# Kernel tuning notes

Hardware: AMD Instinct MI355X
Metric: run time of the kernel (lower is better)

The kernel has to match this reference:

```python
import jax, jax.numpy as jnp
import numpy as np
from jax import lax

B, L, E = 2, 2048, 1024          # batch, seq_len, embed_dim
NL = 2                            # n_layers
DI = 2 * E                        # d_inner (expand=2)
DS = 16                           # d_state
DC = 4                            # d_conv
DTR = (E + 15) // 16              # dt_rank = ceil(d_model/16) = 64


def setup_inputs() -> dict:
    key = jax.random.key(0)
    ks = jax.random.split(key, 12)
    s = 0.02
    inp = {
        "x": jax.random.normal(ks[0], (B, L, E), jnp.float32),
        "pos_embed": jax.random.normal(ks[1], (L, E), jnp.float32) * s,
        "in_proj_w": jax.random.normal(ks[2], (NL, 2 * DI, E), jnp.float32) * s,
        "conv_w": jax.random.normal(ks[3], (NL, DI, DC), jnp.float32) * s,
        "conv_b": jnp.zeros((NL, DI), jnp.float32),
        "x_proj_w": jax.random.normal(ks[4], (NL, DTR + 2 * DS, DI), jnp.float32) * s,
        "dt_proj_w": jax.random.normal(ks[5], (NL, DI, DTR), jnp.float32) * s,
        "dt_bias": jax.random.normal(ks[6], (NL, DI), jnp.float32) * 0.1,
        "A_log": jnp.broadcast_to(jnp.log(jnp.arange(1, DS + 1, dtype=jnp.float32)), (NL, DI, DS)) + 0.0,
        "D_skip": jnp.ones((NL, DI), jnp.float32),
        "out_proj_w": jax.random.normal(ks[7], (NL, E, DI), jnp.float32) * s,
        "norm_w": jnp.ones((NL, E), jnp.float32),
    }
    return inp


def _rmsnorm(x, w, eps=1e-6):
    return x * lax.rsqrt(jnp.mean(x * x, axis=-1, keepdims=True) + eps) * w


def _mamba(h, in_w, cw, cb, xw, dtw, dtb, A_log, Dp, ow):
    # h: (B, L, E)
    xz = jnp.einsum("ble,de->bld", h, in_w)          # (B, L, 2*DI)
    xc, z = jnp.split(xz, 2, axis=-1)                 # each (B, L, DI)
    # causal depthwise conv1d (kernel DC)
    xp = jnp.pad(xc, ((0, 0), (DC - 1, 0), (0, 0)))
    xconv = cb
    acc = jnp.zeros_like(xc)
    for k in range(DC):
        acc = acc + cw[:, k] * xp[:, k:k + xc.shape[1], :]
    xc = jax.nn.silu(acc + cb)
    # input-dependent SSM params
    x_dbl = jnp.einsum("bld,rd->blr", xc, xw)         # (B, L, DTR+2*DS)
    dt, Bm, C = jnp.split(x_dbl, [DTR, DTR + DS], axis=-1)
    delta = jax.nn.softplus(jnp.einsum("blr,dr->bld", dt, dtw) + dtb)  # (B, L, DI)
    A = -jnp.exp(A_log)                               # (DI, DS)

    def step(hst, inp):
        d, bm, c, u = inp                             # (B,DI),(B,DS),(B,DS),(B,DI)
        hst = jnp.exp(d[..., None] * A) * hst + (d * u)[..., None] * bm[:, None, :]
        y = jnp.einsum("bdn,bn->bd", hst, c)
        return hst, y

    h0 = jnp.zeros((h.shape[0], DI, DS), h.dtype)
    _, ys = lax.scan(step, h0, (delta.swapaxes(0, 1), Bm.swapaxes(0, 1),
                                C.swapaxes(0, 1), xc.swapaxes(0, 1)))
    y = ys.swapaxes(0, 1) + xc * Dp                   # (B, L, DI)
    y = y * jax.nn.silu(z)
    return jnp.einsum("bld,ed->ble", y, ow)


def reference(x, pos_embed, in_proj_w, conv_w, conv_b, x_proj_w, dt_proj_w,
              dt_bias, A_log, D_skip, out_proj_w, norm_w):
    h = x + pos_embed[None, :x.shape[1]]
    for i in range(in_proj_w.shape[0]):
        y = _mamba(h, in_proj_w[i], conv_w[i], conv_b[i], x_proj_w[i],
                   dt_proj_w[i], dt_bias[i], A_log[i], D_skip[i], out_proj_w[i])
        h = _rmsnorm(y + h, norm_w[i])
    return h
```

## Files before the change

### kernel.cpp

```cpp
#include <hip/hip_runtime.h>

#define B_   2
#define L_   2048
#define E_   1024
#define NL_  2
#define DI_  2048
#define DS_  16
#define DC_  4
#define DTR_ 64
#define NXD_ 96
#define M_   (B_ * L_)
#define NCH_ 64
#define LC_  32

typedef __attribute__((ext_vector_type(8))) short bf16x8;
typedef __attribute__((ext_vector_type(4))) float f32x4;

__device__ __forceinline__ float bf2f(unsigned short u) {
    return __uint_as_float(((unsigned)u) << 16);
}
__device__ __forceinline__ unsigned short f2bf(float f) {
    unsigned u = __float_as_uint(f);
    u += 0x7fff + ((u >> 16) & 1);
    return (unsigned short)(u >> 16);
}

#define LOG2E_ 1.44269504f
#define LN2_   0.69314718f

__device__ __forceinline__ float sigmoidf_(float x) {
    return __builtin_amdgcn_rcpf(1.f + __builtin_amdgcn_exp2f(-x * LOG2E_));
}
__device__ __forceinline__ float softplusf_(float x) {
    float e = __builtin_amdgcn_exp2f(x * LOG2E_);
    float s = LN2_ * __builtin_amdgcn_logf(1.f + e);
    return x > 15.f ? x : s;
}
__device__ __forceinline__ float expf_(float x) {
    return __builtin_amdgcn_exp2f(x * LOG2E_);
}
__device__ __forceinline__ float ldin(const void* p, size_t i, int isbf) {
    return isbf ? bf2f(((const unsigned short*)p)[i]) : ((const float*)p)[i];
}
__device__ __forceinline__ void gld_lds16(const unsigned short* g, unsigned short* l) {
    __builtin_amdgcn_global_load_lds(
        (const __attribute__((address_space(1))) unsigned int*)g,
        (__attribute__((address_space(3))) unsigned int*)l, 16, 0, 0);
}
__device__ __forceinline__ bf16x8 ds_read128_(unsigned byteoff) {
    bf16x8 r;
    asm volatile("ds_read_b128 %0, %1" : "=&v"(r) : "v"(byteoff));
    return r;
}

__device__ __forceinline__ void expvec(int fast, float dv, const float* a2, float* e) {
    if (fast) {
        float p1 = __builtin_amdgcn_exp2f(dv * a2[0]);
        float p2 = p1 * p1, p4 = p2 * p2, p8 = p4 * p4;
        e[0] = p1;        e[1] = p2;        e[2] = p2 * p1;   e[3] = p4;
        e[4] = p4 * p1;   e[5] = p4 * p2;   e[6] = e[5] * p1; e[7] = p8;
        e[8] = p8 * p1;   e[9] = p8 * p2;   e[10] = e[9] * p1; e[11] = p8 * p4;
        e[12] = e[11] * p1; e[13] = e[11] * p2; e[14] = e[13] * p1; e[15] = p8 * p8;
    } else {
#pragma unroll
        for (int n = 0; n < 16; ++n) e[n] = __builtin_amdgcn_exp2f(dv * a2[n]);
    }
}

__global__ __launch_bounds__(256) void detect_kernel(const unsigned* __restrict__ x,
                                                     int* __restrict__ flags)
{
    __shared__ int cnt;
    if (threadIdx.x == 0) cnt = 0;
    __syncthreads();
    unsigned v = x[threadIdx.x];
    int e = (v >> 7) & 0xFF;
    if (e >= 90 && e <= 140) atomicAdd(&cnt, 1);
    __syncthreads();
    if (threadIdx.x == 0) {
        flags[0] = (cnt >= 192) ? 1 : 0;
        flags[1] = 1;
        flags[2] = 1;
    }
}

__global__ __launch_bounds__(256) void chk_alog(
    const void* __restrict__ alog, int* __restrict__ flags)
{
    int isbf = flags[0];
    int i = blockIdx.x * 256 + threadIdx.x;
    int layer = i / (DI_ * DS_);
    int n = i & (DS_ - 1);
    float a  = -expf_(ldin(alog, i, isbf));
    float a0 = -expf_(ldin(alog, i - n, isbf));
    float want = (n + 1) * a0;
    if (fabsf(a - want) > 0.02f * fabsf(want))
        atomicAnd(&flags[1 + layer], 0);
}

#define WB_IN_  0
#define WB_XW_  4194304
#define WB_DTW_ 4456448
#define WB_OW_  4587520
#define WB_TOT_ 6684672
__global__ __launch_bounds__(256) void cvt_layer_kernel(
    const void* __restrict__ inw, const void* __restrict__ xw,
    const void* __restrict__ dtw, const void* __restrict__ ow,
    int layer, unsigned short* __restrict__ wbuf, const int* __restrict__ flag)
{
    int isbf = *flag;
    int i = blockIdx.x * 256 + threadIdx.x;
    if (isbf && (i < WB_XW_ || i >= WB_DTW_)) return;
    unsigned short v;
    if (i < WB_XW_) {
        v = isbf ? ((const unsigned short*)inw)[(size_t)layer * 2 * DI_ * E_ + i]
                 : f2bf(((const float*)inw)[(size_t)layer * 2 * DI_ * E_ + i]);
    } else if (i < WB_DTW_) {
        int j = i - WB_XW_; int r = j >> 11, k = j & (DI_ - 1);
        v = (r < NXD_)
          ? (isbf ? ((const unsigned short*)xw)[(size_t)layer * NXD_ * DI_ + (size_t)r * DI_ + k]
                  : f2bf(((const float*)xw)[(size_t)layer * NXD_ * DI_ + (size_t)r * DI_ + k]))
          : (unsigned short)0;
    } else if (i < WB_OW_) {
        int j = i - WB_DTW_;
        v = isbf ? ((const unsigned short*)dtw)[(size_t)layer * DI_ * DTR_ + j]
                 : f2bf(((const float*)dtw)[(size_t)layer * DI_ * DTR_ + j]);
    } else {
        int j = i - WB_OW_;
        v = isbf ? ((const unsigned short*)ow)[(size_t)layer * E_ * DI_ + j]
                 : f2bf(((const float*)ow)[(size_t)layer * E_ * DI_ + j]);
    }
    wbuf[i] = v;
}

__global__ __launch_bounds__(256) void add_pos_kernel(
    const void* __restrict__ x, const void* __restrict__ pos,
    float* __restrict__ h, unsigned short* __restrict__ h16,
    const int* __restrict__ flag)
{
    int isbf = *flag;
    int i = blockIdx.x * 256 + threadIdx.x;
    float v = ldin(x, i, isbf) + ldin(pos, i & (L_ * E_ - 1), isbf);
    h[i] = v;
    h16[i] = f2bf(v);
}

__global__ __launch_bounds__(256) void gemm_mfma(
    const unsigned short* __restrict__ A, int lda,
    const unsigned short* __restrict__ W, int ldw,
    void* __restrict__ C, int ldc, int Ksplit, size_t cSliceStride,
    const void* __restrict__ bias, size_t boff,
    void* __restrict__ C2, int ep, const int* __restrict__ flag,
    const unsigned short* __restrict__ Worig)
{
    __shared__ unsigned short As[128 * 64];
    __shared__ unsigned short Bs[128 * 64];
    int isbf = flag ? *flag : 1;
    const unsigned short* Wp = (Worig && isbf) ? Worig : W;
    int tid = threadIdx.x;
    int lane = tid & 63, w = tid >> 6;
    int m0 = blockIdx.x * 128, n0 = blockIdx.y * 128;
    int wm = (w >> 1) * 64, wn = (w & 1) * 64;
    int col = lane & 15, quad = lane >> 4;
    int kstart = blockIdx.z * Ksplit;

    f32x4 acc[4][4];
#pragma unroll
    for (int i = 0; i < 4; ++i)
#pragma unroll
        for (int j = 0; j < 4; ++j)
            acc[i][j] = (f32x4){0.f, 0.f, 0.f, 0.f};

    for (int kt = kstart; kt < kstart + Ksplit; kt += 64) {
#pragma unroll
        for (int i = 0; i < 4; ++i) {
            int seg = i * 4 + w;
            int q = seg * 64 + lane;
            int r = q >> 3, cd = q & 7;
            int cs = cd ^ (r & 7);
            gld_lds16(A + (size_t)(m0 + r) * lda + kt + cs * 8, &As[seg * 512]);
            gld_lds16(Wp + (size_t)(n0 + r) * ldw + kt + cs * 8, &Bs[seg * 512]);
        }
        __syncthreads();
#pragma unroll
        for (int ks = 0; ks < 2; ++ks) {
            bf16x8 af[4], bfr[4];
#pragma unroll
            for (int t = 0; t < 4; ++t) {
                int rowA = wm + t * 16 + col;
                int ca = ks * 4 + quad;
                af[t]  = *(const bf16x8*)&As[rowA * 64 + ((ca ^ (rowA & 7)) * 8)];
                int rowB = wn + t * 16 + col;
                bfr[t] = *(const bf16x8*)&Bs[rowB * 64 + ((ca ^ (rowB & 7)) * 8)];
            }
#pragma unroll
            for (int tm = 0; tm < 4; ++tm)
#pragma unroll
                for (int tn = 0; tn < 4; ++tn)
                    acc[tm][tn] = __builtin_amdgcn_mfma_f32_16x16x32_bf16(
                        af[tm], bfr[tn], acc[tm][tn], 0, 0, 0);
        }
        __syncthreads();
    }

    float* Cp = (float*)C + (size_t)blockIdx.z * cSliceStride;
#pragma unroll
    for (int tm = 0; tm < 4; ++tm)
#pragma unroll
        for (int tn = 0; tn < 4; ++tn)
#pragma unroll
            for (int rg = 0; rg < 4; ++rg) {
                int gm = m0 + wm + tm * 16 + quad * 4 + rg;
                int gn = n0 + wn + tn * 16 + col;
                float v = acc[tm][tn][rg];
                if (ep == 0) {
                    Cp[(size_t)gm * ldc + gn] = v;
                } else {
                    v = softplusf_(v + ldin(bias, boff + gn, isbf));
                    ((unsigned short*)C)[(size_t)gm * ldc + gn] = f2bf(v);
                }
            }
}

template <int KS, int MH, int RB, int CHK>
__device__ __forceinline__ void g8_phase(
    unsigned baseA, unsigned baseB,
    bf16x8 (&af)[4], bf16x8 (&bfr)[4], f32x4 (&acc)[8][4],
    int doStage, int st_t, int st_isB, int st_ks,
    const unsigned short* srcA, const unsigned short* srcW,
    unsigned short* ldsb, int w)
{
    if (RB) {
#pragma unroll
        for (int j = 0; j < 4; ++j)
            bfr[j] = ds_read128_(baseB + j * 2048 + KS * 1024);
    }
#pragma unroll
    for (int f = 0; f < 4; ++f)
        af[f] = ds_read128_(baseA + MH * 8192 + f * 2048 + KS * 1024);
    if (doStage) {
        const unsigned short* s0 = (st_isB ? srcW : srcA)
            + (size_t)w * 16 * E_ + st_t * 64 + st_ks * 32;
        unsigned short* d0 = ldsb + (st_t & 1) * 32768 + st_isB * 16384
            + w * 1024 + st_ks * 512;
        gld_lds16(s0, d0);
        gld_lds16(s0 + (size_t)8 * 16 * E_, d0 + 8 * 1024);
    }
    __builtin_amdgcn_s_barrier();
    asm volatile("s_waitcnt lgkmcnt(0)" ::: "memory");
    __builtin_amdgcn_sched_barrier(0);
    __builtin_amdgcn_s_setprio(1);
#pragma unroll
    for (int f = 0; f < 4; ++f)
#pragma unroll
        for (int j = 0; j < 4; ++j)
            acc[MH * 4 + f][j] = __builtin_amdgcn_mfma_f32_16x16x32_bf16(
                af[f], bfr[j], acc[MH * 4 + f][j], 0, 0, 0);
    __builtin_amdgcn_s_setprio(0);
    if (CHK == 8) { asm volatile("s_waitcnt vmcnt(8)" ::: "memory"); __builtin_amdgcn_sched_barrier(0); }
    if (CHK == 4) { asm volatile("s_waitcnt vmcnt(4)" ::: "memory"); __builtin_amdgcn_sched_barrier(0); }
    if (CHK == 0) { asm volatile("s_waitcnt vmcnt(0)"  ::: "memory"); __builtin_amdgcn_sched_barrier(0); }
    __builtin_amdgcn_s_barrier();
}

__global__ __launch_bounds__(512) void gemm_inproj8(
    const unsigned short* __restrict__ A,
    const unsigned short* __restrict__ Wbuf,
    const unsigned short* __restrict__ Worig,
    const int* __restrict__ flag,
    unsigned short* __restrict__ Cx,
    unsigned short* __restrict__ Cz)
{
    __shared__ unsigned short lds[65536];
    const unsigned short* W = (*flag) ? Worig : Wbuf;
    int tid = threadIdx.x;
    int lane = tid & 63, w = tid >> 6;
    int wr = w >> 2, wc = w & 3;
    int col = lane & 15, quad = lane >> 4;

    int flat = blockIdx.y * 16 + blockIdx.x;
    int nn = (flat & 7) * 32 + (flat >> 3);
    int cch = nn >> 5, wi = nn & 31;
    int bx = (cch & 3) * 4 + (wi & 3);
    int by = (cch >> 2) * 8 + (wi >> 2);
    int m0 = bx * 256, n0 = by * 256;

    const unsigned short* srcA = A + (size_t)(m0 + (lane & 15)) * E_ + (lane >> 4) * 8;
    const unsigned short* srcW = W + (size_t)(n0 + (lane & 15)) * E_ + (lane >> 4) * 8;

    unsigned baseA0 = (unsigned)(wr * 8 * 2048 + quad * 256 + col * 16);
    unsigned baseB0 = (unsigned)(32768 + wc * 4 * 2048 + quad * 256 + col * 16);
    unsigned baseA1 = baseA0 + 65536, baseB1 = baseB0 + 65536;

    f32x4 acc[8][4];
#pragma unroll
    for (int i = 0; i < 8; ++i)
#pragma unroll
        for (int j = 0; j < 4; ++j)
            acc[i][j] = (f32x4){0.f, 0.f, 0.f, 0.f};
    bf16x8 af[4], bfr[4];

#define G8STAGE(t_, isB_, ks_) { \
    const unsigned short* s0 = ((isB_) ? srcW : srcA) + (size_t)w * 16 * E_ + (t_) * 64 + (ks_) * 32; \
    unsigned short* d0 = lds + ((t_) & 1) * 32768 + (isB_) * 16384 + w * 1024 + (ks_) * 512; \
    gld_lds16(s0, d0); gld_lds16(s0 + (size_t)8 * 16 * E_, d0 + 8 * 1024); }

    G8STAGE(0, 0, 0) G8STAGE(0, 1, 0) G8STAGE(0, 0, 1) G8STAGE(0, 1, 1)
    G8STAGE(1, 0, 0) G8STAGE(1, 1, 0)
    asm volatile("s_waitcnt vmcnt(8)" ::: "memory");
    __builtin_amdgcn_sched_barrier(0);
    __builtin_amdgcn_s_barrier();

    for (int i = 0; i < 7; ++i) {
        int t1 = 2 * i + 1, t2 = 2 * i + 2, t3 = 2 * i + 3;
        g8_phase<0,0,1,-1>(baseA0, baseB0, af, bfr, acc, 1, t1, 0, 1, srcA, srcW, lds, w);
        g8_phase<0,1,0, 8>(baseA0, baseB0, af, bfr, acc, 1, t1, 1, 1, srcA, srcW, lds, w);
        g8_phase<1,0,1,-1>(baseA0, baseB0, af, bfr, acc, 1, t2, 0, 0, srcA, srcW, lds, w);
        g8_phase<1,1,0, 8>(baseA0, baseB0, af, bfr, acc, 1, t2, 1, 0, srcA, srcW, lds, w);
        g8_phase<0,0,1,-1>(baseA1, baseB1, af, bfr, acc, 1, t2, 0, 1, srcA, srcW, lds, w);
        g8_phase<0,1,0, 8>(baseA1, baseB1, af, bfr, acc, 1, t2, 1, 1, srcA, srcW, lds, w);
        g8_phase<1,0,1,-1>(baseA1, baseB1, af, bfr, acc, 1, t3, 0, 0, srcA, srcW, lds, w);
        g8_phase<1,1,0, 8>(baseA1, baseB1, af, bfr, acc, 1, t3, 1, 0, srcA, srcW, lds, w);
    }
    g8_phase<0,0,1,-1>(baseA0, baseB0, af, bfr, acc, 1, 15, 0, 1, srcA, srcW, lds, w);
    g8_phase<0,1,0, 8>(baseA0, baseB0, af, bfr, acc, 1, 15, 1, 1, srcA, srcW, lds, w);
    g8_phase<1,0,1,-1>(baseA0, baseB0, af, bfr, acc, 0, 0, 0, 0, srcA, srcW, lds, w);
    g8_phase<1,1,0, 4>(baseA0, baseB0, af, bfr, acc, 0, 0, 0, 0, srcA, srcW, lds, w);
    g8_phase<0,0,1,-1>(baseA1, baseB1, af, bfr, acc, 0, 0, 0, 0, srcA, srcW, lds, w);
    g8_phase<0,1,0, 0>(baseA1, baseB1, af, bfr, acc, 0, 0, 0, 0, srcA, srcW, lds, w);
    g8_phase<1,0,1,-1>(baseA1, baseB1, af, bfr, acc, 0, 0, 0, 0, srcA, srcW, lds, w);
    g8_phase<1,1,0,-1>(baseA1, baseB1, af, bfr, acc, 0, 0, 0, 0, srcA, srcW, lds, w);

    unsigned short* dst = (n0 < DI_) ? Cx : Cz;
    int nb = (n0 < DI_) ? n0 : n0 - DI_;
#pragma unroll
    for (int tm = 0; tm < 8; ++tm)
#pragma unroll
        for (int tn = 0; tn < 4; ++tn)
#pragma unroll
            for (int rg = 0; rg < 4; ++rg) {
                int gm = m0 + wr * 128 + tm * 16 + quad * 4 + rg;
                int gn = nb + wc * 64 + tn * 16 + col;
                dst[(size_t)gm * DI_ + gn] = f2bf(acc[tm][tn][rg]);
            }
#undef G8STAGE
}

__global__ __launch_bounds__(256) void xproj_reduce(
    const float* __restrict__ part, float* __restrict__ xdbl,
    unsigned short* __restrict__ dt16)
{
    int i = blockIdx.x * 256 + threadIdx.x;
    int r = i >> 7, c = i & 127;
    float v = 0.f;
#pragma unroll
    for (int s = 0; s < 8; ++s) v += part[(size_t)s * (M_ * 128) + i];
    if (c < NXD_) xdbl[(size_t)r * NXD_ + c] = v;
    if (c < DTR_) dt16[(size_t)r * DTR_ + c] = f2bf(v);
}

__global__ __launch_bounds__(256) void conv_prep(
    const void* __restrict__ cw, size_t cwoff, const void* __restrict__ cb,
    size_t cboff, float* __restrict__ cwT, float* __restrict__ cbF,
    const int* __restrict__ flag)
{
    int isbf = *flag;
    int d = blockIdx.x * 256 + threadIdx.x;
#pragma unroll
    for (int k = 0; k < DC_; ++k)
        cwT[k * DI_ + d] = ldin(cw, cwoff + (size_t)d * DC_ + k, isbf);
    cbF[d] = ldin(cb, cboff + d, isbf);
}

#define CT_ 4
__global__ __launch_bounds__(256) void conv_silu_v(
    const unsigned short* __restrict__ xcr16, const float* __restrict__ cwT,
    const float* __restrict__ cbF, unsigned short* __restrict__ xc16)
{
    int g = blockIdx.x;
    int bl0 = g * CT_;
    int l0 = bl0 & (L_ - 1);
    int d = threadIdx.x * 8;

    float w[DC_][8], bias[8];
#pragma unroll
    for (int k = 0; k < DC_; ++k) {
        *(float4*)&w[k][0] = *(const float4*)&cwT[k * DI_ + d];
        *(float4*)&w[k][4] = *(const float4*)&cwT[k * DI_ + d + 4];
    }
    *(float4*)&bias[0] = *(const float4*)&cbF[d];
    *(float4*)&bias[4] = *(const float4*)&cbF[d + 4];

    float xr[DC_ - 1 + CT_][8];
#pragma unroll
    for (int r = 0; r < DC_ - 1 + CT_; ++r) {
        int l = l0 - (DC_ - 1) + r;
        if (l >= 0) {
            bf16x8 v = *(const bf16x8*)&xcr16[(size_t)(bl0 - (DC_ - 1) + r) * DI_ + d];
#pragma unroll
            for (int j = 0; j < 8; ++j) xr[r][j] = bf2f((unsigned short)v[j]);
        } else {
#pragma unroll
            for (int j = 0; j < 8; ++j) xr[r][j] = 0.f;
        }
    }

#pragma unroll
    for (int t = 0; t < CT_; ++t) {
        float acc[8];
#pragma unroll
        for (int j = 0; j < 8; ++j) acc[j] = bias[j];
#pragma unroll
        for (int k = 0; k < DC_; ++k)
#pragma unroll
            for (int j = 0; j < 8; ++j)
                acc[j] = fmaf(w[k][j], xr[t + k][j], acc[j]);
        bf16x8 ov;
#pragma unroll
        for (int j = 0; j < 8; ++j) {
            float s = acc[j] * sigmoidf_(acc[j]);
            ov[j] = (short)f2bf(s);
        }
        *(bf16x8*)&xc16[(size_t)(bl0 + t) * DI_ + d] = ov;
    }
}

__global__ __launch_bounds__(256) void scan_part1(
    const unsigned short* __restrict__ dl16, const unsigned short* __restrict__ xc16,
    const float* __restrict__ xdbl,
    const void* __restrict__ A_log, size_t aoff,
    float* __restrict__ sumdbuf, float* __restrict__ scrS,
    const int* __restrict__ flags, int layer)
{
    int isbf = flags[0], fast = flags[1 + layer];
    __shared__ float bs[LC_][16];
    int c = blockIdx.y;
    int b = blockIdx.x >> 3;
    int d = ((blockIdx.x & 7) << 8) + threadIdx.x;
    for (int i = threadIdx.x; i < LC_ * 16; i += 256) {
        int l = i >> 4, n = i & 15;
        bs[l][n] = xdbl[((size_t)b * L_ + c * LC_ + l) * NXD_ + DTR_ + n];
    }
    __syncthreads();
    float a2[16];
#pragma unroll
    for (int n = 0; n < 16; ++n)
        a2[n] = -expf_(ldin(A_log, aoff + (size_t)d * DS_ + n, isbf)) * LOG2E_;
    float s[16] = {};
    float sumd = 0.f;
    const unsigned short* dp = dl16 + ((size_t)b * L_ + c * LC_) * DI_ + d;
    const unsigned short* up = xc16 + ((size_t)b * L_ + c * LC_) * DI_ + d;
    for (int l = 0; l < LC_; ++l) {
        float dv = bf2f(dp[(size_t)l * DI_]);
        float u  = bf2f(up[(size_t)l * DI_]);
        sumd += dv;
        float dvu = dv * u;
        float e[16];
        expvec(fast, dv, a2, e);
        float4 b0 = *(const float4*)&bs[l][0];
        float4 b1 = *(const float4*)&bs[l][4];
        float4 b2 = *(const float4*)&bs[l][8];
        float4 b3 = *(const float4*)&bs[l][12];
        float bv[16] = {b0.x,b0.y,b0.z,b0.w, b1.x,b1.y,b1.z,b1.w,
                        b2.x,b2.y,b2.z,b2.w, b3.x,b3.y,b3.z,b3.w};
#pragma unroll
        for (int n = 0; n < 16; ++n)
            s[n] = fmaf(e[n], s[n], dvu * bv[n]);
    }
    int g = b * DI_ + d;
    sumdbuf[(size_t)c * (B_ * DI_) + g] = sumd;
    size_t base = ((size_t)c * (B_ * DI_) + g) * 16;
#pragma unroll
    for (int q = 0; q < 4; ++q)
        *(float4*)&scrS[base + q * 4] =
            make_float4(s[q*4], s[q*4+1], s[q*4+2], s[q*4+3]);
}

__global__ __launch_bounds__(256) void scan_combine(
    const float* __restrict__ sumdbuf, float* __restrict__ scrS,
    const void* __restrict__ A_log, size_t aoff, const int* __restrict__ flags)
{
    int isbf = flags[0];
    int t = blockIdx.x * 256 + threadIdx.x;
    int g = t >> 4, n = t & 15;
    int d = g & (DI_ - 1);
    float a2 = -expf_(ldin(A_log, aoff + (size_t)d * DS_ + n, isbf)) * LOG2E_;
    float sd[NCH_], sl[NCH_];
#pragma unroll
    for (int c = 0; c < NCH_; ++c) {
        sd[c] = sumdbuf[(size_t)c * (B_ * DI_) + g];
        sl[c] = scrS[(size_t)c * (B_ * DI_ * 16) + t];
    }
    float s = 0.f;
#pragma unroll
    for (int c = 0; c < NCH_; ++c) {
        float P = __builtin_amdgcn_exp2f(a2 * sd[c]);
        float nxt = fmaf(P, s, sl[c]);
        scrS[(size_t)c * (B_ * DI_ * 16) + t] = s;
        s = nxt;
    }
}

__global__ __launch_bounds__(256) void scan_part2(
    const unsigned short* __restrict__ dl16, unsigned short* __restrict__ xc16,
    const float* __restrict__ xdbl, const unsigned short* __restrict__ z,
    const void* __restrict__ A_log, size_t aoff,
    const void* __restrict__ Dskip, size_t doff,
    const float* __restrict__ scrS, const int* __restrict__ flags, int layer)
{
    int isbf = flags[0], fast = flags[1 + layer];
    __shared__ float bs[LC_][32];
    int c = blockIdx.y;
    int b = blockIdx.x >> 3;
    int d = ((blockIdx.x & 7) << 8) + threadIdx.x;
    for (int i = threadIdx.x; i < LC_ * 32; i += 256) {
        int l = i >> 5, n = i & 31;
        bs[l][n] = xdbl[((size_t)b * L_ + c * LC_ + l) * NXD_ + DTR_ + n];
    }
    __syncthreads();
    float a2[16];
#pragma unroll
    for (int n = 0; n < 16; ++n)
        a2[n] = -expf_(ldin(A_log, aoff + (size_t)d * DS_ + n, isbf)) * LOG2E_;
    float Dv = ldin(Dskip, doff + d, isbf);
    int g = b * DI_ + d;
    size_t sbase = ((size_t)c * (B_ * DI_) + g) * 16;
    float s[16];
#pragma unroll
    for (int q = 0; q < 4; ++q) {
        float4 sv = *(const float4*)&scrS[sbase + q * 4];
        s[q*4] = sv.x; s[q*4+1] = sv.y; s[q*4+2] = sv.z; s[q*4+3] = sv.w;
    }

    const unsigned short* dp = dl16 + ((size_t)b * L_ + c * LC_) * DI_ + d;
    unsigned short* up = xc16 + ((size_t)b * L_ + c * LC_) * DI_ + d;
    const unsigned short* zp = z + ((size_t)b * L_ + c * LC_) * DI_ + d;
    for (int l = 0; l < LC_; ++l) {
        float dv = bf2f(dp[(size_t)l * DI_]);
        float u  = bf2f(up[(size_t)l * DI_]);
        float dvu = dv * u;
        float e[16];
        expvec(fast, dv, a2, e);
        float4 b0 = *(const float4*)&bs[l][0];
        float4 b1 = *(const float4*)&bs[l][4];
        float4 b2 = *(const float4*)&bs[l][8];
        float4 b3 = *(const float4*)&bs[l][12];
        float4 c0 = *(const float4*)&bs[l][16];
        float4 c1 = *(const float4*)&bs[l][20];
        float4 c2 = *(const float4*)&bs[l][24];
        float4 c3 = *(const float4*)&bs[l][28];
        float bv[16] = {b0.x,b0.y,b0.z,b0.w, b1.x,b1.y,b1.z,b1.w,
                        b2.x,b2.y,b2.z,b2.w, b3.x,b3.y,b3.z,b3.w};
        float cv[16] = {c0.x,c0.y,c0.z,c0.w, c1.x,c1.y,c1.z,c1.w,
                        c2.x,c2.y,c2.z,c2.w, c3.x,c3.y,c3.z,c3.w};
        float y = 0.f;
#pragma unroll
        for (int n = 0; n < 16; ++n) {
            s[n] = fmaf(e[n], s[n], dvu * bv[n]);
            y = fmaf(s[n], cv[n], y);
        }
        float zv = bf2f(zp[(size_t)l * DI_]);
        up[(size_t)l * DI_] = f2bf((y + u * Dv) * (zv * sigmoidf_(zv)));
    }
}

__global__ __launch_bounds__(256) void rmsnorm_kernel(
    const float* __restrict__ y0, const float* __restrict__ y1,
    float* __restrict__ h, unsigned short* __restrict__ h16,
    const void* __restrict__ nw, size_t nwoff, void* __restrict__ out,
    int write_out, const int* __restrict__ flag)
{
    int isbf = *flag;
    __shared__ float red[4];
    int row = blockIdx.x;
    float* hp = h + (size_t)row * E_;
    float v[4]; float ss = 0.f;
#pragma unroll
    for (int i = 0; i < 4; ++i) {
        int e = threadIdx.x + i * 256;
        size_t idx = (size_t)row * E_ + e;
        v[i] = y0[idx] + y1[idx] + hp[e];
        ss += v[i] * v[i];
    }
#pragma unroll
    for (int off = 1; off < 64; off <<= 1) ss += __shfl_xor(ss, off, 64);
    if ((threadIdx.x & 63) == 0) red[threadIdx.x >> 6] = ss;
    __syncthreads();
    ss = red[0] + red[1] + red[2] + red[3];
    float scale = rsqrtf(ss * (1.f / E_) + 1e-6f);
#pragma unroll
    for (int i = 0; i < 4; ++i) {
        int e = threadIdx.x + i * 256;
        float hv = v[i] * scale * ldin(nw, nwoff + e, isbf);
        hp[e] = hv;
        h16[(size_t)row * E_ + e] = f2bf(hv);
        if (write_out) {
            size_t oi = (size_t)row * E_ + e;
            if (isbf) ((unsigned short*)out)[oi] = f2bf(hv);
            else      ((float*)out)[oi] = hv;
        }
    }
}

extern "C" void kernel_launch(void* const* d_in, const int* in_sizes, int n_in,
                              void* d_out, int out_size, void* d_ws, size_t ws_size,
                              hipStream_t stream)
{
    const void* x    = d_in[0];
    const void* pos  = d_in[1];
    const void* inw  = d_in[2];
    const void* cw   = d_in[3];
    const void* cb   = d_in[4];
    const void* xw   = d_in[5];
    const void* dtw  = d_in[6];
    const void* dtb  = d_in[7];
    const void* alog = d_in[8];
    const void* dsk  = d_in[9];
    const void* ow   = d_in[10];
    const void* nw   = d_in[11];

    float* ws = (float*)d_ws;
    float* h      = ws;
    unsigned short* h16  = (unsigned short*)(ws + 4194304);
    unsigned short* z16  = (unsigned short*)(ws + 6291456);
    unsigned short* xc16 = (unsigned short*)(ws + 10485760);
    float* D      = ws + 14680064;
    float* R      = ws + 23068672;
    float* xdbl   = ws + 27262976;
    unsigned short* dt16 = (unsigned short*)(ws + 27656192);
    float* sumd   = ws + 27787264;
    unsigned short* wbuf = (unsigned short*)(ws + 28049408);
    int* flags    = (int*)(ws + 31391744);

    unsigned short* xcr16 = (unsigned short*)R;
    float* xp_part = R;
    float* scrS    = R;
    unsigned short* dl16 = (unsigned short*)D;
    float* yout0 = D;
    float* yout1 = D + (size_t)M_ * E_;
    float* cwT = sumd;
    float* cbF = sumd + DC_ * DI_;

    detect_kernel<<<1, 256, 0, stream>>>((const unsigned*)x, flags);
    chk_alog<<<NL_ * DI_ * DS_ / 256, 256, 0, stream>>>(alog, flags);
    add_pos_kernel<<<M_ * E_ / 256, 256, 0, stream>>>(x, pos, h, h16, flags);

    for (int layer = 0; layer < NL_; ++layer) {
        const unsigned short* inws = (const unsigned short*)inw + (size_t)layer * 2 * DI_ * E_;
        const unsigned short* dtws = (const unsigned short*)dtw + (size_t)layer * DI_ * DTR_;
        const unsigned short* ows  = (const unsigned short*)ow  + (size_t)layer * E_ * DI_;

        cvt_layer_kernel<<<WB_TOT_ / 256, 256, 0, stream>>>(
            inw, xw, dtw, ow, layer, wbuf, flags);
        conv_prep<<<DI_ / 256, 256, 0, stream>>>(
            cw, (size_t)layer * DI_ * DC_, cb, (size_t)layer * DI_, cwT, cbF, flags);

        gemm_inproj8<<<dim3(M_ / 256, 2 * DI_ / 256, 1), 512, 0, stream>>>(
            h16, wbuf + WB_IN_, inws, flags, xcr16, z16);
        conv_silu_v<<<M_ / CT_, 256, 0, stream>>>(xcr16, cwT, cbF, xc16);
        gemm_mfma<<<dim3(M_ / 128, 1, 8), 256, 0, stream>>>(
            xc16, DI_, wbuf + WB_XW_, DI_, xp_part, 128, DI_ / 8, (size_t)M_ * 128,
            nullptr, 0, nullptr, 0, flags, nullptr);
        xproj_reduce<<<M_ * 128 / 256, 256, 0, stream>>>(xp_part, xdbl, dt16);
        gemm_mfma<<<dim3(M_ / 128, DI_ / 128, 1), 256, 0, stream>>>(
            dt16, DTR_, wbuf + WB_DTW_, DTR_, dl16, DI_, DTR_, 0,
            dtb, (size_t)layer * DI_, nullptr, 2, flags, dtws);
        scan_part1<<<dim3(B_ * DI_ / 256, NCH_), 256, 0, stream>>>(
            dl16, xc16, xdbl, alog, (size_t)layer * DI_ * DS_, sumd, scrS, flags, layer);
        scan_combine<<<B_ * DI_ * DS_ / 256, 256, 0, stream>>>(
            sumd, scrS, alog, (size_t)layer * DI_ * DS_, flags);
        scan_part2<<<dim3(B_ * DI_ / 256, NCH_), 256, 0, stream>>>(
            dl16, xc16, xdbl, z16, alog, (size_t)layer * DI_ * DS_,
            dsk, (size_t)layer * DI_, scrS, flags, layer);
        gemm_mfma<<<dim3(M_ / 128, E_ / 128, 2), 256, 0, stream>>>(
            xc16, DI_, wbuf + WB_OW_, DI_, yout0, E_, DI_ / 2, (size_t)M_ * E_,
            nullptr, 0, nullptr, 0, flags, ows);
        rmsnorm_kernel<<<M_, 256, 0, stream>>>(
            yout0, yout1, h, h16, nw, (size_t)layer * E_, d_out,
            layer == NL_ - 1 ? 1 : 0, flags);
    }
}
```

Baseline: 568.5 us.

## Replace split-K x_proj and out_proj GEMMs with direct full-K kernels, halve scan chunks

The x_proj GEMM used an 8-way split-K into a partial buffer followed by a reduce kernel. It is replaced by a dedicated MFMA kernel that loops over the full K, with one 32-row block per workgroup, and writes xdbl and the bf16 dt copy directly. The out_proj GEMM drops its 2-way split-K, so rmsnorm reads a single partial. The scan chunking also changes from 64 chunks of 32 to 32 chunks of 64. This removes partial-sum traffic and a launch, but gives lower parallelism: 128 blocks for x_proj, 256 for out_proj, and fewer scan blocks.

Measured after the change: 646.6 us. 1.14x slower.

```diff
diff --git a/kernel.cpp b/kernel.cpp
--- a/kernel.cpp
+++ b/kernel.cpp
@@ -10,8 +10,8 @@
 #define DTR_ 64
 #define NXD_ 96
 #define M_   (B_ * L_)
-#define NCH_ 64
-#define LC_  32
+#define NCH_ 32
+#define LC_  64
 
 typedef __attribute__((ext_vector_type(8))) short bf16x8;
 typedef __attribute__((ext_vector_type(4))) float f32x4;
@@ -222,6 +222,73 @@
             }
 }
 
+__global__ __launch_bounds__(256) void gemm_xproj(
+    const unsigned short* __restrict__ A,
+    const unsigned short* __restrict__ W,
+    float* __restrict__ xdbl,
+    unsigned short* __restrict__ dt16)
+{
+    __shared__ unsigned short As[32 * 64];
+    __shared__ unsigned short Bs[128 * 64];
+    int tid = threadIdx.x;
+    int lane = tid & 63, w = tid >> 6;
+    int m0 = blockIdx.x * 32;
+    int col = lane & 15, quad = lane >> 4;
+
+    f32x4 acc[2][2];
+#pragma unroll
+    for (int i = 0; i < 2; ++i)
+#pragma unroll
+        for (int j = 0; j < 2; ++j)
+            acc[i][j] = (f32x4){0.f, 0.f, 0.f, 0.f};
+
+    for (int kt = 0; kt < DI_; kt += 64) {
+        {
+            int r = tid >> 3, cd = tid & 7, cs = cd ^ (r & 7);
+            gld_lds16(A + (size_t)(m0 + r) * DI_ + kt + cs * 8, &As[w * 512]);
+        }
+#pragma unroll
+        for (int i = 0; i < 4; ++i) {
+            int seg = i * 4 + w;
+            int q = seg * 64 + lane;
+            int r = q >> 3, cd = q & 7, cs = cd ^ (r & 7);
+            gld_lds16(W + (size_t)r * DI_ + kt + cs * 8, &Bs[seg * 512]);
+        }
+        __syncthreads();
+#pragma unroll
+        for (int ks = 0; ks < 2; ++ks) {
+            int ca = ks * 4 + quad;
+            bf16x8 af[2], bfr[2];
+#pragma unroll
+            for (int t = 0; t < 2; ++t) {
+                int rowA = t * 16 + col;
+                af[t] = *(const bf16x8*)&As[rowA * 64 + ((ca ^ (rowA & 7)) * 8)];
+                int rowB = w * 32 + t * 16 + col;
+                bfr[t] = *(const bf16x8*)&Bs[rowB * 64 + ((ca ^ (rowB & 7)) * 8)];
+            }
+#pragma unroll
+            for (int tm = 0; tm < 2; ++tm)
+#pragma unroll
+                for (int tn = 0; tn < 2; ++tn)
+                    acc[tm][tn] = __builtin_amdgcn_mfma_f32_16x16x32_bf16(
+                        af[tm], bfr[tn], acc[tm][tn], 0, 0, 0);
+        }
+        __syncthreads();
+    }
+#pragma unroll
+    for (int tm = 0; tm < 2; ++tm)
+#pragma unroll
+        for (int tn = 0; tn < 2; ++tn)
+#pragma unroll
+            for (int rg = 0; rg < 4; ++rg) {
+                int gm = m0 + tm * 16 + quad * 4 + rg;
+                int gn = w * 32 + tn * 16 + col;
+                float v = acc[tm][tn][rg];
+                if (gn < NXD_) xdbl[(size_t)gm * NXD_ + gn] = v;
+                if (gn < DTR_) dt16[(size_t)gm * DTR_ + gn] = f2bf(v);
+            }
+}
+
 template <int KS, int MH, int RB, int CHK>
 __device__ __forceinline__ void g8_phase(
     unsigned baseA, unsigned baseB,
@@ -344,19 +411,6 @@
                 dst[(size_t)gm * DI_ + gn] = f2bf(acc[tm][tn][rg]);
             }
 #undef G8STAGE
-}
-
-__global__ __launch_bounds__(256) void xproj_reduce(
-    const float* __restrict__ part, float* __restrict__ xdbl,
-    unsigned short* __restrict__ dt16)
-{
-    int i = blockIdx.x * 256 + threadIdx.x;
-    int r = i >> 7, c = i & 127;
-    float v = 0.f;
-#pragma unroll
-    for (int s = 0; s < 8; ++s) v += part[(size_t)s * (M_ * 128) + i];
-    if (c < NXD_) xdbl[(size_t)r * NXD_ + c] = v;
-    if (c < DTR_) dt16[(size_t)r * DTR_ + c] = f2bf(v);
 }
 
 __global__ __launch_bounds__(256) void conv_prep(
@@ -565,7 +619,7 @@
 }
 
 __global__ __launch_bounds__(256) void rmsnorm_kernel(
-    const float* __restrict__ y0, const float* __restrict__ y1,
+    const float* __restrict__ y0,
     float* __restrict__ h, unsigned short* __restrict__ h16,
     const void* __restrict__ nw, size_t nwoff, void* __restrict__ out,
     int write_out, const int* __restrict__ flag)
@@ -579,7 +633,7 @@
     for (int i = 0; i < 4; ++i) {
         int e = threadIdx.x + i * 256;
         size_t idx = (size_t)row * E_ + e;
-        v[i] = y0[idx] + y1[idx] + hp[e];
+        v[i] = y0[idx] + hp[e];
         ss += v[i] * v[i];
     }
 #pragma unroll
@@ -633,11 +687,9 @@
     int* flags    = (int*)(ws + 31391744);
 
     unsigned short* xcr16 = (unsigned short*)R;
-    float* xp_part = R;
     float* scrS    = R;
     unsigned short* dl16 = (unsigned short*)D;
     float* yout0 = D;
-    float* yout1 = D + (size_t)M_ * E_;
     float* cwT = sumd;
     float* cbF = sumd + DC_ * DI_;
 
@@ -658,10 +710,8 @@
         gemm_inproj8<<<dim3(M_ / 256, 2 * DI_ / 256, 1), 512, 0, stream>>>(
             h16, wbuf + WB_IN_, inws, flags, xcr16, z16);
         conv_silu_v<<<M_ / CT_, 256, 0, stream>>>(xcr16, cwT, cbF, xc16);
-        gemm_mfma<<<dim3(M_ / 128, 1, 8), 256, 0, stream>>>(
-            xc16, DI_, wbuf + WB_XW_, DI_, xp_part, 128, DI_ / 8, (size_t)M_ * 128,
-            nullptr, 0, nullptr, 0, flags, nullptr);
-        xproj_reduce<<<M_ * 128 / 256, 256, 0, stream>>>(xp_part, xdbl, dt16);
+        gemm_xproj<<<M_ / 32, 256, 0, stream>>>(
+            xc16, wbuf + WB_XW_, xdbl, dt16);
         gemm_mfma<<<dim3(M_ / 128, DI_ / 128, 1), 256, 0, stream>>>(
             dt16, DTR_, wbuf + WB_DTW_, DTR_, dl16, DI_, DTR_, 0,
             dtb, (size_t)layer * DI_, nullptr, 2, flags, dtws);
@@ -672,11 +722,11 @@
         scan_part2<<<dim3(B_ * DI_ / 256, NCH_), 256, 0, stream>>>(
             dl16, xc16, xdbl, z16, alog, (size_t)layer * DI_ * DS_,
             dsk, (size_t)layer * DI_, scrS, flags, layer);
-        gemm_mfma<<<dim3(M_ / 128, E_ / 128, 2), 256, 0, stream>>>(
-            xc16, DI_, wbuf + WB_OW_, DI_, yout0, E_, DI_ / 2, (size_t)M_ * E_,
+        gemm_mfma<<<dim3(M_ / 128, E_ / 128, 1), 256, 0, stream>>>(
+            xc16, DI_, wbuf + WB_OW_, DI_, yout0, E_, DI_, 0,
             nullptr, 0, nullptr, 0, flags, ows);
         rmsnorm_kernel<<<M_, 256, 0, stream>>>(
-            yout0, yout1, h, h16, nw, (size_t)layer * E_, d_out,
+            yout0, h, h16, nw, (size_t)layer * E_, d_out,
             layer == NL_ - 1 ? 1 : 0, flags);
     }
 }
```

## Split SSM state dimension across two half-waves in chunked scan kernels

Applied to the files above, without the earlier changes.

The scan kernels now give each channel two lanes, with the 16 state entries split as 8 per lane, one in each half of a wave. The grid doubles from 16 to 32 blocks per chunk, and the partial outputs are combined with a cross-half shuffle. This halves per-thread register use and serial work to raise occupancy and parallelism. In exchange, dt/u loads are duplicated across the two halves and the output store runs on only half the lanes.

After: 583.3 us. +2.6%, slower.

```diff
diff --git a/kernel.cpp b/kernel.cpp
--- a/kernel.cpp
+++ b/kernel.cpp
@@ -53,17 +53,19 @@
     return r;
 }
 
-__device__ __forceinline__ void expvec(int fast, float dv, const float* a2, float* e) {
+__device__ __forceinline__ void expvec8(int fast, int sub, float dv, float a2r0,
+                                        const float* a2, float* e) {
     if (fast) {
-        float p1 = __builtin_amdgcn_exp2f(dv * a2[0]);
-        float p2 = p1 * p1, p4 = p2 * p2, p8 = p4 * p4;
-        e[0] = p1;        e[1] = p2;        e[2] = p2 * p1;   e[3] = p4;
-        e[4] = p4 * p1;   e[5] = p4 * p2;   e[6] = e[5] * p1; e[7] = p8;
-        e[8] = p8 * p1;   e[9] = p8 * p2;   e[10] = e[9] * p1; e[11] = p8 * p4;
-        e[12] = e[11] * p1; e[13] = e[11] * p2; e[14] = e[13] * p1; e[15] = p8 * p8;
+        float q1 = __builtin_amdgcn_exp2f(dv * a2r0);
+        float q2 = q1 * q1, q4 = q2 * q2, q8 = q4 * q4;
+        e[0] = q1;      e[1] = q2;      e[2] = q2 * q1; e[3] = q4;
+        e[4] = q4 * q1; e[5] = q4 * q2; e[6] = e[5] * q1; e[7] = q8;
+        float m = sub ? q8 : 1.f;
+#pragma unroll
+        for (int j = 0; j < 8; ++j) e[j] *= m;
     } else {
 #pragma unroll
-        for (int n = 0; n < 16; ++n) e[n] = __builtin_amdgcn_exp2f(dv * a2[n]);
+        for (int j = 0; j < 8; ++j) e[j] = __builtin_amdgcn_exp2f(dv * a2[j]);
     }
 }
 
@@ -435,18 +437,22 @@
     int isbf = flags[0], fast = flags[1 + layer];
     __shared__ float bs[LC_][16];
     int c = blockIdx.y;
-    int b = blockIdx.x >> 3;
-    int d = ((blockIdx.x & 7) << 8) + threadIdx.x;
+    int b = blockIdx.x >> 4;
+    int d0 = (blockIdx.x & 15) << 7;
+    int lane = threadIdx.x & 63, w = threadIdx.x >> 6;
+    int sub = (lane >> 5) & 1;
+    int d = d0 + w * 32 + (lane & 31);
     for (int i = threadIdx.x; i < LC_ * 16; i += 256) {
         int l = i >> 4, n = i & 15;
         bs[l][n] = xdbl[((size_t)b * L_ + c * LC_ + l) * NXD_ + DTR_ + n];
     }
     __syncthreads();
-    float a2[16];
-#pragma unroll
-    for (int n = 0; n < 16; ++n)
-        a2[n] = -expf_(ldin(A_log, aoff + (size_t)d * DS_ + n, isbf)) * LOG2E_;
-    float s[16] = {};
+    float a2[8];
+#pragma unroll
+    for (int j = 0; j < 8; ++j)
+        a2[j] = -expf_(ldin(A_log, aoff + (size_t)d * DS_ + sub * 8 + j, isbf)) * LOG2E_;
+    float a2r0 = -expf_(ldin(A_log, aoff + (size_t)d * DS_, isbf)) * LOG2E_;
+    float s[8] = {};
     float sumd = 0.f;
     const unsigned short* dp = dl16 + ((size_t)b * L_ + c * LC_) * DI_ + d;
     const unsigned short* up = xc16 + ((size_t)b * L_ + c * LC_) * DI_ + d;
@@ -455,25 +461,20 @@
         float u  = bf2f(up[(size_t)l * DI_]);
         sumd += dv;
         float dvu = dv * u;
-        float e[16];
-        expvec(fast, dv, a2, e);
-        float4 b0 = *(const float4*)&bs[l][0];
-        float4 b1 = *(const float4*)&bs[l][4];
-        float4 b2 = *(const float4*)&bs[l][8];
-        float4 b3 = *(const float4*)&bs[l][12];
-        float bv[16] = {b0.x,b0.y,b0.z,b0.w, b1.x,b1.y,b1.z,b1.w,
-                        b2.x,b2.y,b2.z,b2.w, b3.x,b3.y,b3.z,b3.w};
-#pragma unroll
-        for (int n = 0; n < 16; ++n)
-            s[n] = fmaf(e[n], s[n], dvu * bv[n]);
+        float e[8];
+        expvec8(fast, sub, dv, a2r0, a2, e);
+        float4 b0 = *(const float4*)&bs[l][sub * 8];
+        float4 b1 = *(const float4*)&bs[l][sub * 8 + 4];
+        float bv[8] = {b0.x, b0.y, b0.z, b0.w, b1.x, b1.y, b1.z, b1.w};
+#pragma unroll
+        for (int j = 0; j < 8; ++j)
+            s[j] = fmaf(e[j], s[j], dvu * bv[j]);
     }
     int g = b * DI_ + d;
-    sumdbuf[(size_t)c * (B_ * DI_) + g] = sumd;
-    size_t base = ((size_t)c * (B_ * DI_) + g) * 16;
-#pragma unroll
-    for (int q = 0; q < 4; ++q)
-        *(float4*)&scrS[base + q * 4] =
-            make_float4(s[q*4], s[q*4+1], s[q*4+2], s[q*4+3]);
+    if (sub == 0) sumdbuf[(size_t)c * (B_ * DI_) + g] = sumd;
+    size_t base = ((size_t)c * (B_ * DI_) + g) * 16 + sub * 8;
+    *(float4*)&scrS[base]     = make_float4(s[0], s[1], s[2], s[3]);
+    *(float4*)&scrS[base + 4] = make_float4(s[4], s[5], s[6], s[7]);
 }
 
 __global__ __launch_bounds__(256) void scan_combine(
@@ -511,25 +512,30 @@
     int isbf = flags[0], fast = flags[1 + layer];
     __shared__ float bs[LC_][32];
     int c = blockIdx.y;
-    int b = blockIdx.x >> 3;
-    int d = ((blockIdx.x & 7) << 8) + threadIdx.x;
+    int b = blockIdx.x >> 4;
+    int d0 = (blockIdx.x & 15) << 7;
+    int lane = threadIdx.x & 63, w = threadIdx.x >> 6;
+    int sub = (lane >> 5) & 1;
+    int d = d0 + w * 32 + (lane & 31);
     for (int i = threadIdx.x; i < LC_ * 32; i += 256) {
         int l = i >> 5, n = i & 31;
         bs[l][n] = xdbl[((size_t)b * L_ + c * LC_ + l) * NXD_ + DTR_ + n];
     }
     __syncthreads();
-    float a2[16];
-#pragma unroll
-    for (int n = 0; n < 16; ++n)
-        a2[n] = -expf_(ldin(A_log, aoff + (size_t)d * DS_ + n, isbf)) * LOG2E_;
+    float a2[8];
+#pragma unroll
+    for (int j = 0; j < 8; ++j)
+        a2[j] = -expf_(ldin(A_log, aoff + (size_t)d * DS_ + sub * 8 + j, isbf)) * LOG2E_;
+    float a2r0 = -expf_(ldin(A_log, aoff + (size_t)d * DS_, isbf)) * LOG2E_;
     float Dv = ldin(Dskip, doff + d, isbf);
     int g = b * DI_ + d;
-    size_t sbase = ((size_t)c * (B_ * DI_) + g) * 16;
-    float s[16];
-#pragma unroll
-    for (int q = 0; q < 4; ++q) {
-        float4 sv = *(const float4*)&scrS[sbase + q * 4];
-        s[q*4] = sv.x; s[q*4+1] = sv.y; s[q*4+2] = sv.z; s[q*4+3] = sv.w;
+    size_t sbase = ((size_t)c * (B_ * DI_) + g) * 16 + sub * 8;
+    float s[8];
+    {
+        float4 sv0 = *(const float4*)&scrS[sbase];
+        float4 sv1 = *(const float4*)&scrS[sbase + 4];
+        s[0] = sv0.x; s[1] = sv0.y; s[2] = sv0.z; s[3] = sv0.w;
+        s[4] = sv1.x; s[5] = sv1.y; s[6] = sv1.z; s[7] = sv1.w;
     }
 
     const unsigned short* dp = dl16 + ((size_t)b * L_ + c * LC_) * DI_ + d;
@@ -539,28 +545,25 @@
         float dv = bf2f(dp[(size_t)l * DI_]);
         float u  = bf2f(up[(size_t)l * DI_]);
         float dvu = dv * u;
-        float e[16];
-        expvec(fast, dv, a2, e);
-        float4 b0 = *(const float4*)&bs[l][0];
-        float4 b1 = *(const float4*)&bs[l][4];
-        float4 b2 = *(const float4*)&bs[l][8];
-        float4 b3 = *(const float4*)&bs[l][12];
-        float4 c0 = *(const float4*)&bs[l][16];
-        float4 c1 = *(const float4*)&bs[l][20];
-        float4 c2 = *(const float4*)&bs[l][24];
-        float4 c3 = *(const float4*)&bs[l][28];
-        float bv[16] = {b0.x,b0.y,b0.z,b0.w, b1.x,b1.y,b1.z,b1.w,
-                        b2.x,b2.y,b2.z,b2.w, b3.x,b3.y,b3.z,b3.w};
-        float cv[16] = {c0.x,c0.y,c0.z,c0.w, c1.x,c1.y,c1.z,c1.w,
-                        c2.x,c2.y,c2.z,c2.w, c3.x,c3.y,c3.z,c3.w};
+        float e[8];
+        expvec8(fast, sub, dv, a2r0, a2, e);
+        float4 b0 = *(const float4*)&bs[l][sub * 8];
+        float4 b1 = *(const float4*)&bs[l][sub * 8 + 4];
+        float4 c0 = *(const float4*)&bs[l][16 + sub * 8];
+        float4 c1 = *(const float4*)&bs[l][16 + sub * 8 + 4];
+        float bv[8] = {b0.x, b0.y, b0.z, b0.w, b1.x, b1.y, b1.z, b1.w};
+        float cv[8] = {c0.x, c0.y, c0.z, c0.w, c1.x, c1.y, c1.z, c1.w};
         float y = 0.f;
 #pragma unroll
-        for (int n = 0; n < 16; ++n) {
-            s[n] = fmaf(e[n], s[n], dvu * bv[n]);
-            y = fmaf(s[n], cv[n], y);
+        for (int j = 0; j < 8; ++j) {
+            s[j] = fmaf(e[j], s[j], dvu * bv[j]);
+            y = fmaf(s[j], cv[j], y);
         }
-        float zv = bf2f(zp[(size_t)l * DI_]);
-        up[(size_t)l * DI_] = f2bf((y + u * Dv) * (zv * sigmoidf_(zv)));
+        y += __shfl_xor(y, 32, 64);
+        if (sub == 0) {
+            float zv = bf2f(zp[(size_t)l * DI_]);
+            up[(size_t)l * DI_] = f2bf((y + u * Dv) * (zv * sigmoidf_(zv)));
+        }
     }
 }
 
@@ -665,11 +668,11 @@
         gemm_mfma<<<dim3(M_ / 128, DI_ / 128, 1), 256, 0, stream>>>(
             dt16, DTR_, wbuf + WB_DTW_, DTR_, dl16, DI_, DTR_, 0,
             dtb, (size_t)layer * DI_, nullptr, 2, flags, dtws);
-        scan_part1<<<dim3(B_ * DI_ / 256, NCH_), 256, 0, stream>>>(
+        scan_part1<<<dim3(32, NCH_), 256, 0, stream>>>(
             dl16, xc16, xdbl, alog, (size_t)layer * DI_ * DS_, sumd, scrS, flags, layer);
         scan_combine<<<B_ * DI_ * DS_ / 256, 256, 0, stream>>>(
             sumd, scrS, alog, (size_t)layer * DI_ * DS_, flags);
-        scan_part2<<<dim3(B_ * DI_ / 256, NCH_), 256, 0, stream>>>(
+        scan_part2<<<dim3(32, NCH_), 256, 0, stream>>>(
             dl16, xc16, xdbl, z16, alog, (size_t)layer * DI_ * DS_,
             dsk, (size_t)layer * DI_, scrS, flags, layer);
         gemm_mfma<<<dim3(M_ / 128, E_ / 128, 2), 256, 0, stream>>>(
```
